# Optimization experiments

Measured on AMD Instinct MI355X. Metric: run time of the kernel, lower is better.

## Reference

```python
import jax, jax.numpy as jnp
import numpy as np

T, D = 32768, 768
NS = NQ = 8192
L = 6


def setup_inputs() -> dict:
    key = jax.random.key(0)
    ks = jax.random.split(key, 8)
    return {
        "tok_support": jax.random.normal(ks[0], (T, D), dtype=jnp.float32),
        "tok_query": jax.random.normal(ks[1], (T, D), dtype=jnp.float32),
        "start_s": jax.random.randint(ks[2], (NS,), 0, T),
        "end_s": jax.random.randint(ks[3], (NS,), 0, T),
        "start_q": jax.random.randint(ks[4], (NQ,), 0, T),
        "end_q": jax.random.randint(ks[5], (NQ,), 0, T),
        "labels_s": jax.random.randint(ks[6], (NS,), 0, L),
        "num_labels": L,
    }


def reference(tok_support, tok_query, start_s, end_s, start_q, end_q, labels_s, num_labels):
    # Span embeddings: concat(start token emb, end token emb)  -> [N, 2D]
    S = jnp.concatenate([tok_support[start_s], tok_support[end_s]], axis=-1)  # [NS, 2D]
    Q = jnp.concatenate([tok_query[start_q], tok_query[end_q]], axis=-1)      # [NQ, 2D]
    # dist[q, s] = -||Q_q - S_s||^2 = 2 Q.S - ||Q||^2 - ||S||^2 (same math, no [NQ,NS,2D] temp)
    dist = (2.0 * (Q @ S.T)
            - jnp.sum(Q * Q, axis=-1, keepdims=True)
            - jnp.sum(S * S, axis=-1)[None, :])  # [NQ, NS]
    NEG = jnp.finfo(dist.dtype).min
    # per-label nearest (max) support distance; num_labels is a small fixed int
    logits = jnp.stack(
        [jnp.max(jnp.where(labels_s == l, dist, NEG), axis=1) for l in range(num_labels)],
        axis=1,
    )  # [NQ, num_labels]
    pred = jnp.argmax(logits, axis=1)
    return logits, pred
```

## Files before the change

kernel.cpp:

```cpp
#include <hip/hip_runtime.h>

#define D_TOK 768
#define NS 8192
#define NQ 8192
#define NL 6
#define KDIM 1536
#define NTN 64
#define NT_K 48

typedef __attribute__((ext_vector_type(4))) float f32x4;
typedef __attribute__((ext_vector_type(8))) short bf16x8;
typedef unsigned int u32;
typedef unsigned short u16;

__device__ __forceinline__ u16 f2bf(float f) {
    u32 u = __float_as_uint(f);
    u32 r = (u + 0x7FFFu + ((u >> 16) & 1u)) >> 16;
    return (u16)r;
}

__global__ __launch_bounds__(256) void prep_kernel(
    const float* __restrict__ tok_support, const float* __restrict__ tok_query,
    const int* __restrict__ start_s, const int* __restrict__ end_s,
    const int* __restrict__ start_q, const int* __restrict__ end_q,
    u16* __restrict__ Qb, u16* __restrict__ Sb,
    float* __restrict__ qn, float* __restrict__ sn) {
    int gw = (blockIdx.x * 256 + threadIdx.x) >> 6;
    int lane = threadIdx.x & 63;
    const float* tok;
    const int *st, *en;
    u16* dst;
    float* nrm;
    int r;
    if (gw < NQ) {
        r = gw; tok = tok_query; st = start_q; en = end_q;
        dst = Qb + (size_t)r * KDIM; nrm = qn + r;
    } else {
        r = gw - NQ; tok = tok_support; st = start_s; en = end_s;
        dst = Sb + (size_t)r * KDIM; nrm = sn + r;
    }
    float ssum = 0.0f;
#pragma unroll
    for (int h = 0; h < 2; ++h) {
        const float4* src4 =
            (const float4*)(tok + (size_t)(h ? en[r] : st[r]) * D_TOK);
        u16* d = dst + h * D_TOK;
#pragma unroll
        for (int it = 0; it < 3; ++it) {
            int i = lane + it * 64;
            float4 v = src4[i];
            ssum += v.x * v.x + v.y * v.y + v.z * v.z + v.w * v.w;
            ushort4 b;
            b.x = f2bf(v.x); b.y = f2bf(v.y); b.z = f2bf(v.z); b.w = f2bf(v.w);
            ((ushort4*)d)[i] = b;
        }
    }
#pragma unroll
    for (int s = 32; s; s >>= 1) ssum += __shfl_xor(ssum, s);
    if (lane == 0) *nrm = ssum;
}

__global__ __launch_bounds__(256) void gemm_kernel(
    const u16* __restrict__ Qb, const u16* __restrict__ Sb,
    const float* __restrict__ qn, const float* __restrict__ sn,
    const int* __restrict__ labels, float* __restrict__ part) {
    __shared__ u16 As[2][128 * 32];
    __shared__ u16 Bs[2][128 * 32];
    __shared__ float red[2][128][NL];

    const int tid = threadIdx.x;
    const int lane = tid & 63;
    const int wid = tid >> 6;
    const int wm = wid >> 1;
    const int wn = wid & 1;
    const int l15 = lane & 15;
    const int lq = lane >> 4;

    const int bid = blockIdx.x;
    const int x = bid & 7;
    const int lid = bid >> 3;
    const int stn = lid >> 6;
    const int inner = lid & 63;
    const int tm = x * 8 + (inner >> 3);
    const int tn = stn * 8 + (inner & 7);
    const int bm = tm * 128;
    const int bn = tn * 128;

    f32x4 acc[4][4] = {};

    const int srow = tid >> 2;
    const int scol = (tid & 3) * 8;
    const u16* gA = Qb + (size_t)(bm + srow) * KDIM + scol;
    const u16* gB = Sb + (size_t)(bn + srow) * KDIM + scol;

#define STAGE(buf, k0)                                                        \
    do {                                                                      \
        __builtin_amdgcn_global_load_lds(                                     \
            (__attribute__((address_space(1))) void*)(u16*)(gA + (k0)),       \
            (__attribute__((address_space(3))) void*)(As[buf] + tid * 8), 16, \
            0, 0);                                                            \
        __builtin_amdgcn_global_load_lds(                                     \
            (__attribute__((address_space(1))) void*)(u16*)(gA + 64 * KDIM +  \
                                                            (k0)),            \
            (__attribute__((address_space(3))) void*)(As[buf] + 2048 +        \
                                                      tid * 8),               \
            16, 0, 0);                                                        \
        __builtin_amdgcn_global_load_lds(                                     \
            (__attribute__((address_space(1))) void*)(u16*)(gB + (k0)),       \
            (__attribute__((address_space(3))) void*)(Bs[buf] + tid * 8), 16, \
            0, 0);                                                            \
        __builtin_amdgcn_global_load_lds(                                     \
            (__attribute__((address_space(1))) void*)(u16*)(gB + 64 * KDIM +  \
                                                            (k0)),            \
            (__attribute__((address_space(3))) void*)(Bs[buf] + 2048 +        \
                                                      tid * 8),               \
            16, 0, 0);                                                        \
    } while (0)

    STAGE(0, 0);
    __syncthreads();
    int cur = 0;
    for (int t = 0; t < NT_K; ++t) {
        if (t + 1 < NT_K) STAGE(cur ^ 1, (t + 1) * 32);
        bf16x8 af[4], bfr[4];
#pragma unroll
        for (int m = 0; m < 4; ++m)
            af[m] = *(const bf16x8*)(As[cur] + (wm * 64 + m * 16 + l15) * 32 +
                                     lq * 8);
#pragma unroll
        for (int n = 0; n < 4; ++n)
            bfr[n] = *(const bf16x8*)(Bs[cur] + (wn * 64 + n * 16 + l15) * 32 +
                                      lq * 8);
#pragma unroll
        for (int m = 0; m < 4; ++m)
#pragma unroll
            for (int n = 0; n < 4; ++n)
                acc[m][n] = __builtin_amdgcn_mfma_f32_16x16x32_bf16(
                    af[m], bfr[n], acc[m][n], 0, 0, 0);
        __syncthreads();
        cur ^= 1;
    }

    float sncol[4];
    int lab[4];
#pragma unroll
    for (int n = 0; n < 4; ++n) {
        int c = bn + wn * 64 + n * 16 + l15;
        sncol[n] = sn[c];
        lab[n] = labels[c];
    }
    const float NEGF = -3.402823466e38f;
#pragma unroll
    for (int m = 0; m < 4; ++m) {
#pragma unroll
        for (int j = 0; j < 4; ++j) {
            int rl = wm * 64 + m * 16 + lq * 4 + j;
            float q2 = qn[bm + rl];
            float lmax[NL];
#pragma unroll
            for (int t = 0; t < NL; ++t) lmax[t] = NEGF;
#pragma unroll
            for (int n = 0; n < 4; ++n) {
                float v = 2.0f * acc[m][n][j] - q2 - sncol[n];
#pragma unroll
                for (int t = 0; t < NL; ++t)
                    lmax[t] = fmaxf(lmax[t], lab[n] == t ? v : NEGF);
            }
#pragma unroll
            for (int t = 0; t < NL; ++t) {
                float v = lmax[t];
                v = fmaxf(v, __shfl_xor(v, 1));
                v = fmaxf(v, __shfl_xor(v, 2));
                v = fmaxf(v, __shfl_xor(v, 4));
                v = fmaxf(v, __shfl_xor(v, 8));
                if (l15 == t) red[wn][rl][t] = v;
            }
        }
    }
    __syncthreads();
    for (int i = tid; i < 128 * NL; i += 256) {
        int r = i / NL, t = i - r * NL;
        float v = fmaxf(red[0][r][t], red[1][r][t]);
        part[((size_t)(bm + r) * NTN + tn) * NL + t] = v;
    }
#undef STAGE
}

__global__ __launch_bounds__(256) void final_kernel(
    const float* __restrict__ part, float* __restrict__ out) {
    int q = (blockIdx.x * 256 + threadIdx.x) >> 6;
    int lane = threadIdx.x & 63;
    const float* p = part + ((size_t)q * NTN + lane) * NL;
    float v[NL];
#pragma unroll
    for (int t = 0; t < NL; ++t) v[t] = p[t];
#pragma unroll
    for (int t = 0; t < NL; ++t) {
#pragma unroll
        for (int s = 32; s; s >>= 1) v[t] = fmaxf(v[t], __shfl_xor(v[t], s));
    }
    if (lane == 0) {
        float best = -3.402823466e38f;
        int bi = 0;
#pragma unroll
        for (int t = 0; t < NL; ++t) {
            out[q * NL + t] = v[t];
            if (v[t] > best) { best = v[t]; bi = t; }
        }
        out[NQ * NL + q] = (float)bi;
    }
}

extern "C" void kernel_launch(void* const* d_in, const int* in_sizes, int n_in,
                              void* d_out, int out_size, void* d_ws,
                              size_t ws_size, hipStream_t stream) {
    const float* tok_support = (const float*)d_in[0];
    const float* tok_query = (const float*)d_in[1];
    const int* start_s = (const int*)d_in[2];
    const int* end_s = (const int*)d_in[3];
    const int* start_q = (const int*)d_in[4];
    const int* end_q = (const int*)d_in[5];
    const int* labels_s = (const int*)d_in[6];

    char* ws = (char*)d_ws;
    u16* Qb = (u16*)ws;
    u16* Sb = (u16*)(ws + 25165824);
    float* qn = (float*)(ws + 50331648);
    float* sn = (float*)(ws + 50364416);
    float* part = (float*)(ws + 50397184);

    prep_kernel<<<dim3((NQ + NS) / 4), dim3(256), 0, stream>>>(
        tok_support, tok_query, start_s, end_s, start_q, end_q, Qb, Sb, qn, sn);
    gemm_kernel<<<dim3(64 * 64), dim3(256), 0, stream>>>(Qb, Sb, qn, sn,
                                                         labels_s, part);
    final_kernel<<<dim3(NQ * 64 / 256), dim3(256), 0, stream>>>(part,
                                                                (float*)d_out);
}
```

Measured before the change: 567.0 us.

## Restructure GEMM into 256x256 tiles with 8 waves and swizzled LDS pipeline

Replaces the 128x128 tile, 4-wave GEMM with a 256x256 tile, 8-wave kernel using a 64-wide K step and XOR-swizzled LDS layout. Global-to-LDS loads for A and B are staggered across two buffers and interleaved with quarter-tile MFMA groups under explicit barriers, vmcnt waits and setprio. The aim is more operand reuse per byte loaded, fewer LDS bank conflicts and better overlap of loads with matrix math. The costs are a large LDS footprint (128 KB), higher register pressure from 32 accumulators per wave, and lower occupancy. The partial-max reduction and final kernel are adapted to 32 column tiles.

```diff
diff --git a/kernel.cpp b/kernel.cpp
--- a/kernel.cpp
+++ b/kernel.cpp
@@ -5,8 +5,10 @@
 #define NQ 8192
 #define NL 6
 #define KDIM 1536
-#define NTN 64
-#define NT_K 48
+#define BM 256
+#define BN 256
+#define NTN 32
+#define NITER 12
 
 typedef __attribute__((ext_vector_type(4))) float f32x4;
 typedef __attribute__((ext_vector_type(8))) short bf16x8;
@@ -60,87 +62,152 @@
     if (lane == 0) *nrm = ssum;
 }
 
-__global__ __launch_bounds__(256) void gemm_kernel(
+__global__ __launch_bounds__(512) void gemm_kernel(
     const u16* __restrict__ Qb, const u16* __restrict__ Sb,
     const float* __restrict__ qn, const float* __restrict__ sn,
     const int* __restrict__ labels, float* __restrict__ part) {
-    __shared__ u16 As[2][128 * 32];
-    __shared__ u16 Bs[2][128 * 32];
-    __shared__ float red[2][128][NL];
+    __shared__ char lds[131072];
+    u16* As = (u16*)lds;
+    u16* Bs = (u16*)(lds + 65536);
+    const char* Ab = (const char*)lds;
+    const char* Bb = (const char*)(lds + 65536);
 
     const int tid = threadIdx.x;
     const int lane = tid & 63;
     const int wid = tid >> 6;
-    const int wm = wid >> 1;
-    const int wn = wid & 1;
+    const int wm = wid >> 2;
+    const int wn = wid & 3;
     const int l15 = lane & 15;
     const int lq = lane >> 4;
 
     const int bid = blockIdx.x;
     const int x = bid & 7;
     const int lid = bid >> 3;
-    const int stn = lid >> 6;
-    const int inner = lid & 63;
-    const int tm = x * 8 + (inner >> 3);
-    const int tn = stn * 8 + (inner & 7);
-    const int bm = tm * 128;
-    const int bn = tn * 128;
-
-    f32x4 acc[4][4] = {};
-
-    const int srow = tid >> 2;
-    const int scol = (tid & 3) * 8;
-    const u16* gA = Qb + (size_t)(bm + srow) * KDIM + scol;
-    const u16* gB = Sb + (size_t)(bn + srow) * KDIM + scol;
-
-#define STAGE(buf, k0)                                                        \
-    do {                                                                      \
-        __builtin_amdgcn_global_load_lds(                                     \
-            (__attribute__((address_space(1))) void*)(u16*)(gA + (k0)),       \
-            (__attribute__((address_space(3))) void*)(As[buf] + tid * 8), 16, \
-            0, 0);                                                            \
-        __builtin_amdgcn_global_load_lds(                                     \
-            (__attribute__((address_space(1))) void*)(u16*)(gA + 64 * KDIM +  \
-                                                            (k0)),            \
-            (__attribute__((address_space(3))) void*)(As[buf] + 2048 +        \
-                                                      tid * 8),               \
-            16, 0, 0);                                                        \
-        __builtin_amdgcn_global_load_lds(                                     \
-            (__attribute__((address_space(1))) void*)(u16*)(gB + (k0)),       \
-            (__attribute__((address_space(3))) void*)(Bs[buf] + tid * 8), 16, \
-            0, 0);                                                            \
-        __builtin_amdgcn_global_load_lds(                                     \
-            (__attribute__((address_space(1))) void*)(u16*)(gB + 64 * KDIM +  \
-                                                            (k0)),            \
-            (__attribute__((address_space(3))) void*)(Bs[buf] + 2048 +        \
-                                                      tid * 8),               \
-            16, 0, 0);                                                        \
-    } while (0)
-
-    STAGE(0, 0);
-    __syncthreads();
-    int cur = 0;
-    for (int t = 0; t < NT_K; ++t) {
-        if (t + 1 < NT_K) STAGE(cur ^ 1, (t + 1) * 32);
-        bf16x8 af[4], bfr[4];
-#pragma unroll
-        for (int m = 0; m < 4; ++m)
-            af[m] = *(const bf16x8*)(As[cur] + (wm * 64 + m * 16 + l15) * 32 +
-                                     lq * 8);
-#pragma unroll
-        for (int n = 0; n < 4; ++n)
-            bfr[n] = *(const bf16x8*)(Bs[cur] + (wn * 64 + n * 16 + l15) * 32 +
-                                      lq * 8);
-#pragma unroll
-        for (int m = 0; m < 4; ++m)
-#pragma unroll
-            for (int n = 0; n < 4; ++n)
-                acc[m][n] = __builtin_amdgcn_mfma_f32_16x16x32_bf16(
-                    af[m], bfr[n], acc[m][n], 0, 0, 0);
-        __syncthreads();
-        cur ^= 1;
-    }
-
+    const int tm = x * 4 + (lid & 3);
+    const int tn = lid >> 2;
+    const int bm = tm * BM;
+    const int bn = tn * BN;
+
+    int grow[4], gcol[4];
+#pragma unroll
+    for (int j = 0; j < 4; ++j) {
+        int p = j * 8192 + tid * 16;
+        int q = p ^ (((p >> 9) & 1) << 5);
+        grow[j] = q >> 7;
+        gcol[j] = (q & 127) >> 1;
+    }
+    const u16* gA = Qb + (size_t)bm * KDIM;
+    const u16* gB = Sb + (size_t)bn * KDIM;
+
+    const int swz = ((l15 >> 2) & 1) << 5;
+    const int aBase = ((wm * 128 + l15) * 128 + lq * 16) ^ swz;
+    const int bBase = ((wn * 64 + l15) * 128 + lq * 16) ^ swz;
+
+    f32x4 acc[8][4] = {};
+    bf16x8 af[4][2], bf[2][2];
+
+#define STG(dst, g, b, t)                                                     \
+    do {                                                                      \
+        _Pragma("unroll") for (int j = 0; j < 4; ++j) {                       \
+            __builtin_amdgcn_global_load_lds(                                 \
+                (__attribute__((address_space(1))) void*)(u16*)(              \
+                    (g) + (size_t)grow[j] * KDIM + (t) * 64 + gcol[j]),       \
+                (__attribute__((address_space(3))) void*)(                    \
+                    (dst) + (b) * 16384 + j * 4096 + tid * 8),                \
+                16, 0, 0);                                                    \
+        }                                                                     \
+    } while (0)
+
+#define READ_A(b, m0)                                                         \
+    do {                                                                      \
+        _Pragma("unroll") for (int i = 0; i < 4; ++i)                         \
+            _Pragma("unroll") for (int kk = 0; kk < 2; ++kk)                  \
+                af[i][kk] = *(const bf16x8*)(Ab + (b) * 32768 + aBase +       \
+                                             ((m0) + i) * 2048 + kk * 64);    \
+    } while (0)
+
+#define READ_B(b, n0)                                                         \
+    do {                                                                      \
+        _Pragma("unroll") for (int jj = 0; jj < 2; ++jj)                      \
+            _Pragma("unroll") for (int kk = 0; kk < 2; ++kk)                  \
+                bf[jj][kk] = *(const bf16x8*)(Bb + (b) * 32768 + bBase +      \
+                                              ((n0) + jj) * 2048 + kk * 64);  \
+    } while (0)
+
+#define MFMA_Q(m0, n0)                                                        \
+    do {                                                                      \
+        __builtin_amdgcn_s_setprio(1);                                        \
+        _Pragma("unroll") for (int i = 0; i < 4; ++i)                         \
+            _Pragma("unroll") for (int jj = 0; jj < 2; ++jj)                  \
+                _Pragma("unroll") for (int kk = 0; kk < 2; ++kk)              \
+                    acc[(m0) + i][(n0) + jj] =                                \
+                        __builtin_amdgcn_mfma_f32_16x16x32_bf16(              \
+                            af[i][kk], bf[jj][kk], acc[(m0) + i][(n0) + jj],  \
+                            0, 0, 0);                                         \
+        __builtin_amdgcn_s_setprio(0);                                        \
+    } while (0)
+
+#define BAR __builtin_amdgcn_s_barrier()
+#define HANDOFF(N)                                                            \
+    do {                                                                      \
+        __builtin_amdgcn_sched_barrier(0);                                    \
+        asm volatile("s_waitcnt vmcnt(" #N ")" ::: "memory");                 \
+        __builtin_amdgcn_s_barrier();                                         \
+        __builtin_amdgcn_sched_barrier(0);                                    \
+    } while (0)
+
+    STG(As, gA, 0, 0);
+    STG(Bs, gB, 0, 0);
+    STG(As, gA, 1, 1);
+    HANDOFF(4);
+
+#pragma unroll 1
+    for (int it = 0; it < NITER; ++it) {
+        const int more = (it < NITER - 1);
+        READ_A(0, 0);
+        READ_B(0, 0);
+        STG(Bs, gB, 1, 2 * it + 1);
+        BAR;
+        MFMA_Q(0, 0);
+        BAR;
+        READ_B(0, 2);
+        BAR;
+        MFMA_Q(0, 2);
+        BAR;
+        READ_A(0, 4);
+        READ_B(0, 0);
+        BAR;
+        MFMA_Q(4, 0);
+        BAR;
+        READ_B(0, 2);
+        if (more) STG(As, gA, 0, 2 * it + 2);
+        BAR;
+        MFMA_Q(4, 2);
+        if (more) { HANDOFF(4); } else { HANDOFF(0); }
+        READ_A(1, 0);
+        READ_B(1, 0);
+        if (more) STG(Bs, gB, 0, 2 * it + 2);
+        BAR;
+        MFMA_Q(0, 0);
+        BAR;
+        READ_B(1, 2);
+        BAR;
+        MFMA_Q(0, 2);
+        BAR;
+        READ_A(1, 4);
+        READ_B(1, 0);
+        BAR;
+        MFMA_Q(4, 0);
+        BAR;
+        READ_B(1, 2);
+        if (more) STG(As, gA, 1, 2 * it + 3);
+        BAR;
+        MFMA_Q(4, 2);
+        if (more) { HANDOFF(4); } else { HANDOFF(0); }
+    }
+
+    float* red = (float*)lds;
+    const float NEGF = -3.402823466e38f;
     float sncol[4];
     int lab[4];
 #pragma unroll
@@ -149,13 +216,12 @@
         sncol[n] = sn[c];
         lab[n] = labels[c];
     }
-    const float NEGF = -3.402823466e38f;
-#pragma unroll
-    for (int m = 0; m < 4; ++m) {
+#pragma unroll
+    for (int m = 0; m < 8; ++m) {
 #pragma unroll
         for (int j = 0; j < 4; ++j) {
-            int rl = wm * 64 + m * 16 + lq * 4 + j;
-            float q2 = qn[bm + rl];
+            int rl = m * 16 + lq * 4 + j;
+            float q2 = qn[bm + wm * 128 + rl];
             float lmax[NL];
 #pragma unroll
             for (int t = 0; t < NL; ++t) lmax[t] = NEGF;
@@ -173,34 +239,48 @@
                 v = fmaxf(v, __shfl_xor(v, 2));
                 v = fmaxf(v, __shfl_xor(v, 4));
                 v = fmaxf(v, __shfl_xor(v, 8));
-                if (l15 == t) red[wn][rl][t] = v;
+                if (l15 == t)
+                    red[((wm * 128 + rl) * 4 + wn) * NL + t] = v;
             }
         }
     }
     __syncthreads();
-    for (int i = tid; i < 128 * NL; i += 256) {
-        int r = i / NL, t = i - r * NL;
-        float v = fmaxf(red[0][r][t], red[1][r][t]);
-        part[((size_t)(bm + r) * NTN + tn) * NL + t] = v;
-    }
-#undef STAGE
+    for (int i = tid; i < 256 * NL; i += 512) {
+        int rf = i / NL, t = i - rf * NL;
+        float v = fmaxf(
+            fmaxf(red[(rf * 4 + 0) * NL + t], red[(rf * 4 + 1) * NL + t]),
+            fmaxf(red[(rf * 4 + 2) * NL + t], red[(rf * 4 + 3) * NL + t]));
+        part[(size_t)(bm + rf) * (NTN * NL) + tn * NL + t] = v;
+    }
+#undef STG
+#undef READ_A
+#undef READ_B
+#undef MFMA_Q
+#undef BAR
+#undef HANDOFF
 }
 
 __global__ __launch_bounds__(256) void final_kernel(
     const float* __restrict__ part, float* __restrict__ out) {
     int q = (blockIdx.x * 256 + threadIdx.x) >> 6;
     int lane = threadIdx.x & 63;
-    const float* p = part + ((size_t)q * NTN + lane) * NL;
+    const float NEGF = -3.402823466e38f;
     float v[NL];
-#pragma unroll
-    for (int t = 0; t < NL; ++t) v[t] = p[t];
+    if (lane < NTN) {
+        const float* p = part + ((size_t)q * NTN + lane) * NL;
+#pragma unroll
+        for (int t = 0; t < NL; ++t) v[t] = p[t];
+    } else {
+#pragma unroll
+        for (int t = 0; t < NL; ++t) v[t] = NEGF;
+    }
 #pragma unroll
     for (int t = 0; t < NL; ++t) {
 #pragma unroll
         for (int s = 32; s; s >>= 1) v[t] = fmaxf(v[t], __shfl_xor(v[t], s));
     }
     if (lane == 0) {
-        float best = -3.402823466e38f;
+        float best = NEGF;
         int bi = 0;
 #pragma unroll
         for (int t = 0; t < NL; ++t) {
@@ -231,7 +311,7 @@
 
     prep_kernel<<<dim3((NQ + NS) / 4), dim3(256), 0, stream>>>(
         tok_support, tok_query, start_s, end_s, start_q, end_q, Qb, Sb, qn, sn);
-    gemm_kernel<<<dim3(64 * 64), dim3(256), 0, stream>>>(Qb, Sb, qn, sn,
+    gemm_kernel<<<dim3(32 * 32), dim3(512), 0, stream>>>(Qb, Sb, qn, sn,
                                                          labels_s, part);
     final_kernel<<<dim3(NQ * 64 / 256), dim3(256), 0, stream>>>(part,
                                                                 (float*)d_out);
```

New measurement: 543.5 us. -4.1%, faster.
